# Kernel optimization log

Hardware: AMD Instinct MI355X
Metric: run time of the kernel (lower is better)

The kernel has to match this reference:

```python
import jax, jax.numpy as jnp
import numpy as np

IN_FEATURES = [32, 32]
OUT_FEATURES = [64, 64]
RANKS = [16, 16, 16, 16]


def _make_cores(key):
    dims = IN_FEATURES + OUT_FEATURES
    ranks = RANKS
    # init scale as in the torch module
    var = 2 ** (1.0 / len(dims)) / np.prod(np.power(np.array(ranks) + np.array(IN_FEATURES + IN_FEATURES), 1.0 / len(dims)))
    ub = float(np.sqrt(3.0 * var))
    ranks_ext = [ranks[-1]] + list(ranks)
    cores = []
    for i in range(len(dims)):
        key, k = jax.random.split(key)
        cores.append(jax.random.uniform(k, (ranks_ext[i], dims[i], ranks_ext[i + 1]), jnp.float32, -ub, ub))
    return cores, key


def setup_inputs() -> dict:
    key = jax.random.key(0)
    cores, key = _make_cores(key)
    key, kx, kb = jax.random.split(key, 3)
    x = jax.random.normal(kx, (8192, int(np.prod(IN_FEATURES))), jnp.float32)
    bias = jax.random.normal(kb, (int(np.prod(OUT_FEATURES)),), jnp.float32)
    return {"x": x, "core0": cores[0], "core1": cores[1], "core2": cores[2], "core3": cores[3], "bias": bias}


def reference(x, core0, core1, core2, core3, bias):
    # Tensor-ring contraction to build the dense weight, then linear.
    # core shapes: (16,32,16), (16,32,16), (16,64,16), (16,64,16)
    w = jnp.tensordot(core0, core1, axes=([2], [0]))        # (r, i0, i1, r)
    w = jnp.tensordot(w, core2, axes=([3], [0]))            # (r, i0, i1, o0, r)
    # last core: contract w's trailing rank with core axis 0 AND w's leading
    # rank with core's trailing rank (closes the ring) -> (i0, i1, o0, o1)
    w = jnp.tensordot(w, core3, axes=([4, 0], [0, 2]))
    d_out = int(np.prod(OUT_FEATURES))
    w = w.reshape(d_out, -1)                                # (4096, 1024)
    return x @ w.T + bias
```

## Files before the change

### kernel.cpp

```cpp
#include <hip/hip_runtime.h>
#include <hip/hip_bf16.h>
#include <stdint.h>

typedef unsigned short ushort_t;
typedef __attribute__((ext_vector_type(8))) short short8;
typedef __attribute__((ext_vector_type(4))) float floatx4;

__device__ __forceinline__ ushort_t f2bf(float f) {
    union { float f; unsigned u; } v; v.f = f;
    unsigned r = v.u + 0x7fffu + ((v.u >> 16) & 1u);
    return (ushort_t)(r >> 16);
}

__device__ __forceinline__ void async16(ushort_t* lds, const ushort_t* g) {
    __builtin_amdgcn_global_load_lds(
        (const __attribute__((address_space(1))) unsigned int*)g,
        (__attribute__((address_space(3))) unsigned int*)lds, 16, 0, 0);
}

#define WAIT_VMCNT(n) asm volatile("s_waitcnt vmcnt(" #n ")" ::: "memory")
__device__ __forceinline__ void barrier_nodrain() {
    asm volatile("" ::: "memory");
    __builtin_amdgcn_s_barrier();
    asm volatile("" ::: "memory");
}

__global__ __launch_bounds__(256) void prep_all(const float* __restrict__ x,
                                                const float* __restrict__ c0,
                                                const float* __restrict__ c1,
                                                const float* __restrict__ c2,
                                                const float* __restrict__ c3,
                                                ushort_t* __restrict__ Xb,
                                                ushort_t* __restrict__ A2b,
                                                ushort_t* __restrict__ Bg1) {
    const int b = blockIdx.x, t = threadIdx.x;
    if (b < 8192) {
        int i = b * 256 + t;
        float4 v = ((const float4*)x)[i];
        ushort4 r;
        r.x = f2bf(v.x); r.y = f2bf(v.y); r.z = f2bf(v.z); r.w = f2bf(v.w);
        ((ushort4*)Xb)[i] = r;
    } else if (b < 9216) {
        int id = (b - 8192) * 256 + t;
        int k = id & 255, ii = id >> 8;
        int r0 = k >> 4, r2 = k & 15;
        int i0 = ii >> 5, i1 = ii & 31;
        const float* p0 = c0 + (r0 * 32 + i0) * 16;
        const float* p1 = c1 + i1 * 16 + r2;
        float s = 0.f;
#pragma unroll
        for (int r1 = 0; r1 < 16; r1++) s += p0[r1] * p1[r1 * 512];
        A2b[id] = f2bf(s);
    } else {
        int id = (b - 9216) * 256 + t;
        int c = id & 1023, n = id >> 10;
        int bq = n >> 8, k = n & 255;
        int r0 = k >> 4, r2 = k & 15;
        int o0 = bq * 16 + (c >> 6), o1 = c & 63;
        const float* p2 = c2 + (r2 * 64 + o0) * 16;
        const float* p3 = c3 + o1 * 16 + r0;
        float s = 0.f;
#pragma unroll
        for (int r3 = 0; r3 < 16; r3++) s += p2[r3] * p3[r3 * 1024];
        Bg1[id] = f2bf(s);
    }
}

__global__ __launch_bounds__(256) void gemm1_u(const ushort_t* __restrict__ Xb,
                                               const ushort_t* __restrict__ Bg1,
                                               ushort_t* __restrict__ U) {
    __shared__ ushort_t As[2][128 * 32];
    __shared__ ushort_t Bs[2][128 * 32];
    const int t = threadIdx.x;
    const unsigned orig = blockIdx.x;
    const unsigned wg = (orig & 7) * 64 + (orig >> 3);
    const int row0 = (int)(wg >> 3) * 128;
    const int col0 = (int)(wg & 7) * 128;
    const int w = t >> 6, l = t & 63;
    const int wm = w >> 1, wn = w & 1;
    const int quad = l >> 4, ln = l & 15;

    floatx4 acc[4][4] = {};

    const ushort_t* aSrc = Xb  + (size_t)(row0 + (t >> 2)) * 1024 + (t & 3) * 8;
    const ushort_t* bSrc = Bg1 + (size_t)(col0 + (t >> 2)) * 1024 + (t & 3) * 8;

    async16(&As[0][t * 8],        aSrc);
    async16(&As[0][2048 + t * 8], aSrc + 64 * 1024);
    async16(&Bs[0][t * 8],        bSrc);
    async16(&Bs[0][2048 + t * 8], bSrc + 64 * 1024);

    int cur = 0;
#pragma unroll 2
    for (int kk = 32; kk < 1024; kk += 32, cur ^= 1) {
        async16(&As[cur ^ 1][t * 8],        aSrc + kk);
        async16(&As[cur ^ 1][2048 + t * 8], aSrc + 64 * 1024 + kk);
        async16(&Bs[cur ^ 1][t * 8],        bSrc + kk);
        async16(&Bs[cur ^ 1][2048 + t * 8], bSrc + 64 * 1024 + kk);

        WAIT_VMCNT(4);
        barrier_nodrain();

        short8 a[4], b[4];
#pragma unroll
        for (int ti = 0; ti < 4; ti++)
            a[ti] = *(const short8*)&As[cur][(wm * 64 + ti * 16 + ln) * 32 + quad * 8];
#pragma unroll
        for (int tj = 0; tj < 4; tj++)
            b[tj] = *(const short8*)&Bs[cur][(wn * 64 + tj * 16 + ln) * 32 + quad * 8];
#pragma unroll
        for (int ti = 0; ti < 4; ti++)
#pragma unroll
            for (int tj = 0; tj < 4; tj++)
                acc[ti][tj] = __builtin_amdgcn_mfma_f32_16x16x32_bf16(
                    a[ti], b[tj], acc[ti][tj], 0, 0, 0);

        barrier_nodrain();
    }
    WAIT_VMCNT(0);
    barrier_nodrain();
    {
        short8 a[4], b[4];
#pragma unroll
        for (int ti = 0; ti < 4; ti++)
            a[ti] = *(const short8*)&As[cur][(wm * 64 + ti * 16 + ln) * 32 + quad * 8];
#pragma unroll
        for (int tj = 0; tj < 4; tj++)
            b[tj] = *(const short8*)&Bs[cur][(wn * 64 + tj * 16 + ln) * 32 + quad * 8];
#pragma unroll
        for (int ti = 0; ti < 4; ti++)
#pragma unroll
            for (int tj = 0; tj < 4; tj++)
                acc[ti][tj] = __builtin_amdgcn_mfma_f32_16x16x32_bf16(
                    a[ti], b[tj], acc[ti][tj], 0, 0, 0);
    }

#pragma unroll
    for (int tj = 0; tj < 4; tj++) {
        const int n = col0 + wn * 64 + tj * 16 + ln;
#pragma unroll
        for (int ti = 0; ti < 4; ti++) {
            const int m = row0 + wm * 64 + ti * 16 + quad * 4;
#pragma unroll
            for (int r = 0; r < 4; r++)
                U[(size_t)(m + r) * 1024 + n] = f2bf(acc[ti][tj][r]);
        }
    }
}

__global__ __launch_bounds__(256) void gemm2_tr(const ushort_t* __restrict__ U,
                                                const ushort_t* __restrict__ A2b,
                                                const float* __restrict__ bias,
                                                float* __restrict__ out) {
    __shared__ ushort_t Us[2][4][64 * 32];
    const int t = threadIdx.x;
    const unsigned orig = blockIdx.x;
    const unsigned wg = (orig & 7) * 256 + (orig >> 3);
    const int jt = (int)(wg & 15), mt = (int)(wg >> 4);
    const int row0 = mt * 64;
    const int a0 = jt * 64;
    const int w = t >> 6, l = t & 63;
    const int wm = w >> 1, wn = w & 1;
    const int quad = l >> 4, ln = l & 15;

    short8 a2f[2][8];
#pragma unroll
    for (int tj = 0; tj < 2; tj++) {
        const ushort_t* ap = A2b + (size_t)(a0 + wn * 32 + tj * 16 + ln) * 256 + quad * 8;
#pragma unroll
        for (int s = 0; s < 8; s++)
            a2f[tj][s] = *(const short8*)&ap[s * 32];
    }

    floatx4 acc[4][2][2] = {};

    const ushort_t* uSrc = U + (size_t)(row0 + (t >> 2)) * 1024 + (t & 3) * 8;

#pragma unroll
    for (int b = 0; b < 4; b++)
        async16(&Us[0][b][t * 8], uSrc + b * 256);

    int cur = 0;
#pragma unroll
    for (int kk8 = 1; kk8 < 8; kk8++, cur ^= 1) {
#pragma unroll
        for (int b = 0; b < 4; b++)
            async16(&Us[cur ^ 1][b][t * 8], uSrc + b * 256 + kk8 * 32);

        WAIT_VMCNT(4);
        barrier_nodrain();

#pragma unroll
        for (int b = 0; b < 4; b++) {
            short8 au[2];
#pragma unroll
            for (int ti = 0; ti < 2; ti++)
                au[ti] = *(const short8*)&Us[cur][b][(wm * 32 + ti * 16 + ln) * 32 + quad * 8];
#pragma unroll
            for (int ti = 0; ti < 2; ti++)
#pragma unroll
                for (int tj = 0; tj < 2; tj++)
                    acc[b][ti][tj] = __builtin_amdgcn_mfma_f32_16x16x32_bf16(
                        au[ti], a2f[tj][kk8 - 1], acc[b][ti][tj], 0, 0, 0);
        }
        barrier_nodrain();
    }
    WAIT_VMCNT(0);
    barrier_nodrain();
#pragma unroll
    for (int b = 0; b < 4; b++) {
        short8 au[2];
#pragma unroll
        for (int ti = 0; ti < 2; ti++)
            au[ti] = *(const short8*)&Us[cur][b][(wm * 32 + ti * 16 + ln) * 32 + quad * 8];
#pragma unroll
        for (int ti = 0; ti < 2; ti++)
#pragma unroll
            for (int tj = 0; tj < 2; tj++)
                acc[b][ti][tj] = __builtin_amdgcn_mfma_f32_16x16x32_bf16(
                    au[ti], a2f[tj][7], acc[b][ti][tj], 0, 0, 0);
    }

#pragma unroll
    for (int tj = 0; tj < 2; tj++) {
        const int a = a0 + wn * 32 + tj * 16 + ln;
        const float4 bv = ((const float4*)bias)[a];
#pragma unroll
        for (int ti = 0; ti < 2; ti++) {
            const int m = row0 + wm * 32 + ti * 16 + quad * 4;
#pragma unroll
            for (int r = 0; r < 4; r++) {
                float4 o;
                o.x = acc[0][ti][tj][r] + bv.x;
                o.y = acc[1][ti][tj][r] + bv.y;
                o.z = acc[2][ti][tj][r] + bv.z;
                o.w = acc[3][ti][tj][r] + bv.w;
                *(float4*)&out[(size_t)(m + r) * 4096 + (size_t)a * 4] = o;
            }
        }
    }
}

extern "C" void kernel_launch(void* const* d_in, const int* in_sizes, int n_in,
                              void* d_out, int out_size, void* d_ws, size_t ws_size,
                              hipStream_t stream) {
    const float* x    = (const float*)d_in[0];
    const float* c0   = (const float*)d_in[1];
    const float* c1   = (const float*)d_in[2];
    const float* c2   = (const float*)d_in[3];
    const float* c3   = (const float*)d_in[4];
    const float* bias = (const float*)d_in[5];
    float* out = (float*)d_out;

    char* ws = (char*)d_ws;
    ushort_t* Xb  = (ushort_t*)out;
    ushort_t* U   = (ushort_t*)ws;
    ushort_t* A2b = (ushort_t*)(ws + (16u << 20));
    ushort_t* Bg1 = (ushort_t*)(ws + (17u << 20));

    hipLaunchKernelGGL(prep_all, dim3(13312), dim3(256), 0, stream,
                       x, c0, c1, c2, c3, Xb, A2b, Bg1);
    hipLaunchKernelGGL(gemm1_u, dim3(512), dim3(256), 0, stream, Xb, Bg1, U);
    hipLaunchKernelGGL(gemm2_tr, dim3(2048), dim3(256), 0, stream, U, A2b, bias, out);
}
```

Measured before the change: 236.4 us.

## Triple-buffer LDS loads in both GEMMs and halve gemm1 M-tile

Both GEMM kernels move from double- to triple-buffered async global-to-LDS loads, keeping two stages in flight with adjusted vmcnt waits so loads overlap compute more deeply. gemm1 also shrinks its row tile from 128 to 64 and doubles the grid to 1024 blocks, which spreads work across more CUs but lowers per-block data reuse and raises B-tile reload traffic. The extra LDS buffer may reduce occupancy.

```diff
diff --git a/kernel.cpp b/kernel.cpp
--- a/kernel.cpp
+++ b/kernel.cpp
@@ -69,78 +69,77 @@
 __global__ __launch_bounds__(256) void gemm1_u(const ushort_t* __restrict__ Xb,
                                                const ushort_t* __restrict__ Bg1,
                                                ushort_t* __restrict__ U) {
-    __shared__ ushort_t As[2][128 * 32];
-    __shared__ ushort_t Bs[2][128 * 32];
+    __shared__ ushort_t As[3 * 64 * 32];
+    __shared__ ushort_t Bs[3 * 128 * 32];
     const int t = threadIdx.x;
     const unsigned orig = blockIdx.x;
-    const unsigned wg = (orig & 7) * 64 + (orig >> 3);
-    const int row0 = (int)(wg >> 3) * 128;
+    const unsigned wg = (orig & 7) * 128 + (orig >> 3);
+    const int row0 = (int)(wg >> 3) * 64;
     const int col0 = (int)(wg & 7) * 128;
     const int w = t >> 6, l = t & 63;
     const int wm = w >> 1, wn = w & 1;
     const int quad = l >> 4, ln = l & 15;
 
-    floatx4 acc[4][4] = {};
+    floatx4 acc[2][4] = {};
 
     const ushort_t* aSrc = Xb  + (size_t)(row0 + (t >> 2)) * 1024 + (t & 3) * 8;
     const ushort_t* bSrc = Bg1 + (size_t)(col0 + (t >> 2)) * 1024 + (t & 3) * 8;
 
-    async16(&As[0][t * 8],        aSrc);
-    async16(&As[0][2048 + t * 8], aSrc + 64 * 1024);
-    async16(&Bs[0][t * 8],        bSrc);
-    async16(&Bs[0][2048 + t * 8], bSrc + 64 * 1024);
-
-    int cur = 0;
-#pragma unroll 2
-    for (int kk = 32; kk < 1024; kk += 32, cur ^= 1) {
-        async16(&As[cur ^ 1][t * 8],        aSrc + kk);
-        async16(&As[cur ^ 1][2048 + t * 8], aSrc + 64 * 1024 + kk);
-        async16(&Bs[cur ^ 1][t * 8],        bSrc + kk);
-        async16(&Bs[cur ^ 1][2048 + t * 8], bSrc + 64 * 1024 + kk);
-
-        WAIT_VMCNT(4);
+    async16(&As[0 * 2048 + t * 8], aSrc);
+    async16(&Bs[0 * 4096 + t * 8], bSrc);
+    async16(&Bs[0 * 4096 + 2048 + t * 8], bSrc + 64 * 1024);
+    async16(&As[1 * 2048 + t * 8], aSrc + 32);
+    async16(&Bs[1 * 4096 + t * 8], bSrc + 32);
+    async16(&Bs[1 * 4096 + 2048 + t * 8], bSrc + 64 * 1024 + 32);
+
+#define G1_COMPUTE(CB)                                                          \
+    {                                                                           \
+        const int aOff = (CB) * 2048, bOff = (CB) * 4096;                       \
+        short8 a[2], b[4];                                                      \
+        _Pragma("unroll")                                                       \
+        for (int ti = 0; ti < 2; ti++)                                          \
+            a[ti] = *(const short8*)&As[aOff + (wm * 32 + ti * 16 + ln) * 32 + quad * 8]; \
+        _Pragma("unroll")                                                       \
+        for (int tj = 0; tj < 4; tj++)                                          \
+            b[tj] = *(const short8*)&Bs[bOff + (wn * 64 + tj * 16 + ln) * 32 + quad * 8]; \
+        _Pragma("unroll")                                                       \
+        for (int ti = 0; ti < 2; ti++)                                          \
+            _Pragma("unroll")                                                   \
+            for (int tj = 0; tj < 4; tj++)                                      \
+                acc[ti][tj] = __builtin_amdgcn_mfma_f32_16x16x32_bf16(          \
+                    a[ti], b[tj], acc[ti][tj], 0, 0, 0);                        \
+    }
+
+    int cb = 0, wb = 2;
+#pragma unroll 3
+    for (int s = 0; s < 30; ++s) {
+        const int kkw = (s + 2) * 32;
+        async16(&As[wb * 2048 + t * 8], aSrc + kkw);
+        async16(&Bs[wb * 4096 + t * 8], bSrc + kkw);
+        async16(&Bs[wb * 4096 + 2048 + t * 8], bSrc + 64 * 1024 + kkw);
+        WAIT_VMCNT(6);
         barrier_nodrain();
-
-        short8 a[4], b[4];
-#pragma unroll
-        for (int ti = 0; ti < 4; ti++)
-            a[ti] = *(const short8*)&As[cur][(wm * 64 + ti * 16 + ln) * 32 + quad * 8];
-#pragma unroll
-        for (int tj = 0; tj < 4; tj++)
-            b[tj] = *(const short8*)&Bs[cur][(wn * 64 + tj * 16 + ln) * 32 + quad * 8];
-#pragma unroll
-        for (int ti = 0; ti < 4; ti++)
-#pragma unroll
-            for (int tj = 0; tj < 4; tj++)
-                acc[ti][tj] = __builtin_amdgcn_mfma_f32_16x16x32_bf16(
-                    a[ti], b[tj], acc[ti][tj], 0, 0, 0);
-
+        G1_COMPUTE(cb);
         barrier_nodrain();
-    }
+        cb = (cb == 2) ? 0 : cb + 1;
+        wb = (wb == 2) ? 0 : wb + 1;
+    }
+    WAIT_VMCNT(3);
+    barrier_nodrain();
+    G1_COMPUTE(cb);
+    barrier_nodrain();
+    cb = (cb == 2) ? 0 : cb + 1;
     WAIT_VMCNT(0);
     barrier_nodrain();
-    {
-        short8 a[4], b[4];
-#pragma unroll
-        for (int ti = 0; ti < 4; ti++)
-            a[ti] = *(const short8*)&As[cur][(wm * 64 + ti * 16 + ln) * 32 + quad * 8];
-#pragma unroll
-        for (int tj = 0; tj < 4; tj++)
-            b[tj] = *(const short8*)&Bs[cur][(wn * 64 + tj * 16 + ln) * 32 + quad * 8];
-#pragma unroll
-        for (int ti = 0; ti < 4; ti++)
-#pragma unroll
-            for (int tj = 0; tj < 4; tj++)
-                acc[ti][tj] = __builtin_amdgcn_mfma_f32_16x16x32_bf16(
-                    a[ti], b[tj], acc[ti][tj], 0, 0, 0);
-    }
+    G1_COMPUTE(cb);
+#undef G1_COMPUTE
 
 #pragma unroll
     for (int tj = 0; tj < 4; tj++) {
         const int n = col0 + wn * 64 + tj * 16 + ln;
 #pragma unroll
-        for (int ti = 0; ti < 4; ti++) {
-            const int m = row0 + wm * 64 + ti * 16 + quad * 4;
+        for (int ti = 0; ti < 2; ti++) {
+            const int m = row0 + wm * 32 + ti * 16 + quad * 4;
 #pragma unroll
             for (int r = 0; r < 4; r++)
                 U[(size_t)(m + r) * 1024 + n] = f2bf(acc[ti][tj][r]);
@@ -152,7 +151,7 @@
                                                 const ushort_t* __restrict__ A2b,
                                                 const float* __restrict__ bias,
                                                 float* __restrict__ out) {
-    __shared__ ushort_t Us[2][4][64 * 32];
+    __shared__ ushort_t Us[3][4][64 * 32];
     const int t = threadIdx.x;
     const unsigned orig = blockIdx.x;
     const unsigned wg = (orig & 7) * 256 + (orig >> 3);
@@ -179,46 +178,38 @@
 #pragma unroll
     for (int b = 0; b < 4; b++)
         async16(&Us[0][b][t * 8], uSrc + b * 256);
-
-    int cur = 0;
-#pragma unroll
-    for (int kk8 = 1; kk8 < 8; kk8++, cur ^= 1) {
-#pragma unroll
-        for (int b = 0; b < 4; b++)
-            async16(&Us[cur ^ 1][b][t * 8], uSrc + b * 256 + kk8 * 32);
-
-        WAIT_VMCNT(4);
+#pragma unroll
+    for (int b = 0; b < 4; b++)
+        async16(&Us[1][b][t * 8], uSrc + b * 256 + 32);
+
+#pragma unroll
+    for (int s = 0; s < 8; s++) {
+        if (s < 6) {
+            const int wb = (s + 2) % 3;
+#pragma unroll
+            for (int b = 0; b < 4; b++)
+                async16(&Us[wb][b][t * 8], uSrc + b * 256 + (s + 2) * 32);
+        }
+        if (s < 6)      WAIT_VMCNT(8);
+        else if (s == 6) WAIT_VMCNT(4);
+        else             WAIT_VMCNT(0);
         barrier_nodrain();
 
+        const int cb = s % 3;
 #pragma unroll
         for (int b = 0; b < 4; b++) {
             short8 au[2];
 #pragma unroll
             for (int ti = 0; ti < 2; ti++)
-                au[ti] = *(const short8*)&Us[cur][b][(wm * 32 + ti * 16 + ln) * 32 + quad * 8];
+                au[ti] = *(const short8*)&Us[cb][b][(wm * 32 + ti * 16 + ln) * 32 + quad * 8];
 #pragma unroll
             for (int ti = 0; ti < 2; ti++)
 #pragma unroll
                 for (int tj = 0; tj < 2; tj++)
                     acc[b][ti][tj] = __builtin_amdgcn_mfma_f32_16x16x32_bf16(
-                        au[ti], a2f[tj][kk8 - 1], acc[b][ti][tj], 0, 0, 0);
-        }
-        barrier_nodrain();
-    }
-    WAIT_VMCNT(0);
-    barrier_nodrain();
-#pragma unroll
-    for (int b = 0; b < 4; b++) {
-        short8 au[2];
-#pragma unroll
-        for (int ti = 0; ti < 2; ti++)
-            au[ti] = *(const short8*)&Us[cur][b][(wm * 32 + ti * 16 + ln) * 32 + quad * 8];
-#pragma unroll
-        for (int ti = 0; ti < 2; ti++)
-#pragma unroll
-            for (int tj = 0; tj < 2; tj++)
-                acc[b][ti][tj] = __builtin_amdgcn_mfma_f32_16x16x32_bf16(
-                    au[ti], a2f[tj][7], acc[b][ti][tj], 0, 0, 0);
+                        au[ti], a2f[tj][s], acc[b][ti][tj], 0, 0, 0);
+        }
+        if (s < 7) barrier_nodrain();
     }
 
 #pragma unroll
@@ -260,6 +251,6 @@
 
     hipLaunchKernelGGL(prep_all, dim3(13312), dim3(256), 0, stream,
                        x, c0, c1, c2, c3, Xb, A2b, Bg1);
-    hipLaunchKernelGGL(gemm1_u, dim3(512), dim3(256), 0, stream, Xb, Bg1, U);
+    hipLaunchKernelGGL(gemm1_u, dim3(1024), dim3(256), 0, stream, Xb, Bg1, U);
     hipLaunchKernelGGL(gemm2_tr, dim3(2048), dim3(256), 0, stream, U, A2b, bias, out);
 }
```

Result: slower. 245.6 us (+3.9%).
